# Optimization experiments

Measured on AMD Instinct MI355X. Metric: run time of the kernel, lower is better.

Reference implementation:

```python
import jax, jax.numpy as jnp
import numpy as np

HEADS = 8
DIM_HEAD = 64


def setup_inputs() -> dict:
    key = jax.random.key(0)
    k1, k2, k3 = jax.random.split(key, 3)
    B, C, L = 8, 512, 8192
    hidden = HEADS * DIM_HEAD  # 512
    x = jax.random.normal(k1, (B, C, L), dtype=jnp.float32)
    W_qkv = jax.random.normal(k2, (3 * hidden, C), dtype=jnp.float32) * (1.0 / np.sqrt(C))
    W_out = jax.random.normal(k3, (C, hidden), dtype=jnp.float32) * (1.0 / np.sqrt(hidden))
    b_out = jnp.zeros((C,), dtype=jnp.float32)
    return {"x": x, "W_qkv": W_qkv, "W_out": W_out, "b_out": b_out}


def reference(x, W_qkv, W_out, b_out):
    b, c, l = x.shape
    h, d = HEADS, DIM_HEAD
    # pointwise conv1d == channel matmul: [3*h*d, c] x [b, c, l] -> [b, 3*h*d, l]
    qkv = jnp.einsum('oc,bcl->bol', W_qkv, x)
    q, k, v = jnp.split(qkv, 3, axis=1)
    q = q.reshape(b, h, d, l)
    k = jax.nn.softmax(k.reshape(b, h, d, l), axis=-1)
    v = v.reshape(b, h, d, l)
    # context = k @ v^T : [b,h,d,d]
    context = jnp.einsum('bhdl,bhel->bhde', k, v)
    # out = context^T @ q : [b,h,e,l]
    out = jnp.einsum('bhde,bhdl->bhel', context, q)
    out = out.reshape(b, h * d, l)
    # to_out pointwise conv with bias
    return jnp.einsum('ch,bhl->bcl', W_out, out) + b_out[None, :, None]
```

## Files before the change

### kernel.cpp

```cpp
#include <hip/hip_runtime.h>
#include <hip/hip_bf16.h>

typedef unsigned short u16;
typedef __attribute__((ext_vector_type(8))) short s16x8;
typedef __attribute__((ext_vector_type(4))) float f32x4;

__device__ __forceinline__ u16 f2bf(float f) {
  union { float f; unsigned u; } v; v.f = f;
  unsigned r = (v.u + 0x7fffu + ((v.u >> 16) & 1u)) >> 16;
  return (u16)r;
}
__device__ __forceinline__ float bf2f(u16 u) {
  union { unsigned u; float f; } v; v.u = ((unsigned)u) << 16;
  return v.f;
}
__device__ __forceinline__ void gld_lds16(const void* g, void* l) {
  __builtin_amdgcn_global_load_lds(
      (const __attribute__((address_space(1))) void*)g,
      (__attribute__((address_space(3))) void*)l, 16, 0, 0);
}
__device__ __forceinline__ s16x8 dsr128(const u16* p) {
  s16x8 r;
  asm volatile("ds_read_b128 %0, %1"
               : "=v"(r)
               : "v"((const __attribute__((address_space(3))) u16*)p));
  return r;
}

__global__ void prep_w(const float* __restrict__ Wqkv, const float* __restrict__ Woutf,
                       u16* __restrict__ Wkv, u16* __restrict__ WqT, u16* __restrict__ Wout) {
  int i = blockIdx.x * 256 + threadIdx.x;
  Wkv[i] = f2bf(Wqkv[262144 + i]);
  if (i < 262144) {
    int c = i >> 9, o = i & 511;
    WqT[i]  = f2bf(Wqkv[o * 512 + c]);
    Wout[i] = f2bf(Woutf[i]);
  }
}

__global__ __launch_bounds__(256) void prep_x(const float* __restrict__ x, u16* __restrict__ xt) {
  __shared__ float t[32][33];
  int l0 = blockIdx.x * 32, c0 = blockIdx.y * 32;
  size_t b = blockIdx.z;
  int tid = threadIdx.x;
  int r = tid >> 3, q = tid & 7;
  const float4 v = *(const float4*)(x + (b * 512 + c0 + r) * 8192 + l0 + q * 4);
  t[r][q * 4 + 0] = v.x; t[r][q * 4 + 1] = v.y;
  t[r][q * 4 + 2] = v.z; t[r][q * 4 + 3] = v.w;
  __syncthreads();
  ushort4 o;
  o.x = f2bf(t[q * 4 + 0][r]); o.y = f2bf(t[q * 4 + 1][r]);
  o.z = f2bf(t[q * 4 + 2][r]); o.w = f2bf(t[q * 4 + 3][r]);
  *(ushort4*)(xt + (b * 8192 + l0 + r) * 512 + c0 + q * 4) = o;
}

__global__ __launch_bounds__(256) void gemm_bt(
    const u16* __restrict__ A, size_t sA,
    const u16* __restrict__ BT, size_t sB,
    u16* __restrict__ Cv, size_t sC,
    int N, int K)
{
  __shared__ u16 lsa[128 * 32];
  __shared__ u16 lsb[128 * 32];
  int tid = threadIdx.x, wid = tid >> 6, lane = tid & 63;
  int m0 = blockIdx.y << 7, n0 = blockIdx.x << 7;
  const u16* Ab = A + (size_t)blockIdx.z * sA;
  const u16* Bb = BT + (size_t)blockIdx.z * sB;
  int fr = lane & 15, kg = lane >> 4;
  int wr = wid >> 1, wc = wid & 1;
  int f0 = tid, f1 = tid + 256;
  const u16* pA0 = Ab + (size_t)(m0 + (f0 >> 2)) * K + (f0 & 3) * 8;
  const u16* pA1 = Ab + (size_t)(m0 + (f1 >> 2)) * K + (f1 & 3) * 8;
  const u16* pB0 = Bb + (size_t)(n0 + (f0 >> 2)) * K + (f0 & 3) * 8;
  const u16* pB1 = Bb + (size_t)(n0 + (f1 >> 2)) * K + (f1 & 3) * 8;
  u16* dA0 = &lsa[wid * 512];
  u16* dA1 = &lsa[(wid + 4) * 512];
  u16* dB0 = &lsb[wid * 512];
  u16* dB1 = &lsb[(wid + 4) * 512];
  f32x4 acc[4][4] = {};
  for (int kt = 0; kt < K; kt += 32) {
    gld_lds16(pA0, dA0); gld_lds16(pA1, dA1);
    gld_lds16(pB0, dB0); gld_lds16(pB1, dB1);
    pA0 += 32; pA1 += 32; pB0 += 32; pB1 += 32;
    __syncthreads();
    s16x8 af[4], bf_[4];
#pragma unroll
    for (int mi = 0; mi < 4; ++mi)
      af[mi] = *(const s16x8*)&lsa[(wr * 64 + mi * 16 + fr) * 32 + kg * 8];
#pragma unroll
    for (int ni = 0; ni < 4; ++ni)
      bf_[ni] = *(const s16x8*)&lsb[(wc * 64 + ni * 16 + fr) * 32 + kg * 8];
#pragma unroll
    for (int mi = 0; mi < 4; ++mi)
#pragma unroll
      for (int ni = 0; ni < 4; ++ni)
        acc[mi][ni] = __builtin_amdgcn_mfma_f32_16x16x32_bf16(af[mi], bf_[ni], acc[mi][ni], 0, 0, 0);
    __syncthreads();
  }
  int r0 = m0 + wr * 64 + kg * 4;
  int c0 = n0 + wc * 64 + fr;
  u16* C = Cv + (size_t)blockIdx.z * sC;
#pragma unroll
  for (int mi = 0; mi < 4; ++mi)
#pragma unroll
    for (int ni = 0; ni < 4; ++ni)
#pragma unroll
      for (int j = 0; j < 4; ++j)
        C[(size_t)(r0 + mi * 16 + j) * N + (c0 + ni * 16)] = f2bf(acc[mi][ni][j]);
}

template <int OUTF>
__global__ __launch_bounds__(256, 3) void gemm128(
    const u16* __restrict__ A, size_t sA,
    const u16* __restrict__ BT, size_t sB,
    void* __restrict__ Cv, size_t sC,
    const float* __restrict__ bias,
    int Mt, int Nt)
{
  __shared__ u16 lsa[3][4096];
  __shared__ u16 lsb[3][4096];
  const int tid = threadIdx.x, wid = tid >> 6, lane = tid & 63;
  const int fr = lane & 15, kg = lane >> 4;
  const int wr = wid >> 1, wc = wid & 1;

  const int nwg = (int)gridDim.x;
  const int bx = (int)blockIdx.x;
  const int id = (bx & 7) * (nwg >> 3) + (bx >> 3);
  const int my = id % Mt;
  const int t2 = id / Mt;
  const int nx = t2 % Nt;
  const int z  = t2 / Nt;
  const int m0 = my << 7, n0 = nx << 7;
  const u16* Ab = A + (size_t)z * sA;
  const u16* Bb = BT + (size_t)z * sB;

  const int P0 = tid, P1 = tid + 256;
  int b2_, s_, t_;
  b2_ = P0 >> 3; s_ = P0 & 7; t_ = (s_ - b2_) & 7;
  const size_t g0 = (size_t)((b2_ << 1) + (t_ >> 2)) * 512 + (t_ & 3) * 8;
  b2_ = P1 >> 3; s_ = P1 & 7; t_ = (s_ - b2_) & 7;
  const size_t g1 = (size_t)((b2_ << 1) + (t_ >> 2)) * 512 + (t_ & 3) * 8;
  const u16* paG0 = Ab + (size_t)m0 * 512 + g0;
  const u16* paG1 = Ab + (size_t)m0 * 512 + g1;
  const u16* pbG0 = Bb + (size_t)n0 * 512 + g0;
  const u16* pbG1 = Bb + (size_t)n0 * 512 + g1;

  int aoff[4], boff[4];
#pragma unroll
  for (int i = 0; i < 4; ++i) {
    int ra = wr * 64 + i * 16 + fr;
    aoff[i] = (ra >> 1) * 64 + ((((ra & 1) << 2) + kg + (ra >> 1)) & 7) * 8;
    int rb = wc * 64 + i * 16 + fr;
    boff[i] = (rb >> 1) * 64 + ((((rb & 1) << 2) + kg + (rb >> 1)) & 7) * 8;
  }

  auto stage = [&](int sl, int kt) {
    gld_lds16(paG0 + kt, &lsa[sl][P0 * 8]);
    gld_lds16(paG1 + kt, &lsa[sl][P1 * 8]);
    gld_lds16(pbG0 + kt, &lsb[sl][P0 * 8]);
    gld_lds16(pbG1 + kt, &lsb[sl][P1 * 8]);
  };

  f32x4 acc[4][4] = {};
  stage(0, 0);
  stage(1, 32);
#pragma unroll
  for (int k = 0; k < 16; ++k) {
    if (k < 14) stage((k + 2) % 3, (k + 2) * 32);
    if (k < 14)      { asm volatile("s_waitcnt vmcnt(8)" ::: "memory"); }
    else if (k == 14){ asm volatile("s_waitcnt vmcnt(4)" ::: "memory"); }
    else             { asm volatile("s_waitcnt vmcnt(0)" ::: "memory"); }
    __builtin_amdgcn_s_barrier();
    s16x8 af[4], bf_[4];
    const u16* la = lsa[k % 3];
    const u16* lb = lsb[k % 3];
#pragma unroll
    for (int mi = 0; mi < 4; ++mi) af[mi] = dsr128(la + aoff[mi]);
#pragma unroll
    for (int ni = 0; ni < 4; ++ni) bf_[ni] = dsr128(lb + boff[ni]);
    asm volatile("s_waitcnt lgkmcnt(0)" ::: "memory");
    __builtin_amdgcn_sched_barrier(0);
    __builtin_amdgcn_s_setprio(1);
#pragma unroll
    for (int mi = 0; mi < 4; ++mi)
#pragma unroll
      for (int ni = 0; ni < 4; ++ni)
        acc[mi][ni] = __builtin_amdgcn_mfma_f32_16x16x32_bf16(af[mi], bf_[ni], acc[mi][ni], 0, 0, 0);
    __builtin_amdgcn_s_setprio(0);
    __builtin_amdgcn_s_barrier();
  }

  const int r0 = m0 + wr * 64 + kg * 4;
  const int c0 = n0 + wc * 64 + fr;
  if (OUTF == 0) {
    u16* C = (u16*)Cv + (size_t)z * sC;
#pragma unroll
    for (int mi = 0; mi < 4; ++mi)
#pragma unroll
      for (int ni = 0; ni < 4; ++ni)
#pragma unroll
        for (int j = 0; j < 4; ++j)
          C[(size_t)(r0 + mi * 16 + j) * 8192 + (c0 + ni * 16)] = f2bf(acc[mi][ni][j]);
  } else {
    float* C = (float*)Cv + (size_t)z * sC;
#pragma unroll
    for (int mi = 0; mi < 4; ++mi)
#pragma unroll
      for (int j = 0; j < 4; ++j) {
        float bv = bias[r0 + mi * 16 + j];
#pragma unroll
        for (int ni = 0; ni < 4; ++ni)
          C[(size_t)(r0 + mi * 16 + j) * 8192 + (c0 + ni * 16)] = acc[mi][ni][j] + bv;
      }
  }
}

#define NSPLIT 16
#define SLICE  512
__global__ __launch_bounds__(256) void ctx_partial(const u16* __restrict__ kv,
                                                   float* __restrict__ E, float* __restrict__ Z) {
  int s = blockIdx.x, h = blockIdx.y, b = blockIdx.z;
  int tid = threadIdx.x, wid = tid >> 6, lane = tid & 63;
  int fr = lane & 15, kg = lane >> 4;
  const u16* kbase = kv + ((size_t)b * 1024 + h * 64) * 8192;
  const u16* vbase = kbase + (size_t)512 * 8192;
  int d = wid * 16 + fr;
  const u16* krow = kbase + (size_t)d * 8192 + s * SLICE + kg * 8;
  f32x4 acc[4] = {};
  float z = 0.f;
  for (int l = 0; l < SLICE; l += 32) {
    s16x8 kf = *(const s16x8*)(krow + l);
    s16x8 pf;
#pragma unroll
    for (int j = 0; j < 8; ++j) {
      float p = __expf(bf2f((u16)kf[j]));
      z += p;
      pf[j] = (short)f2bf(p);
    }
#pragma unroll
    for (int ni = 0; ni < 4; ++ni) {
      int e = ni * 16 + fr;
      const s16x8 vf = *(const s16x8*)(vbase + (size_t)e * 8192 + s * SLICE + kg * 8 + l);
      acc[ni] = __builtin_amdgcn_mfma_f32_16x16x32_bf16(pf, vf, acc[ni], 0, 0, 0);
    }
  }
  z += __shfl_xor(z, 16);
  z += __shfl_xor(z, 32);
  size_t bh = (size_t)(b * 8 + h);
  if (kg == 0) atomicAdd(&Z[bh * 64 + d], z);
  float* Eb = E + bh * 4096;
#pragma unroll
  for (int ni = 0; ni < 4; ++ni)
#pragma unroll
    for (int j = 0; j < 4; ++j)
      atomicAdd(&Eb[(wid * 16 + kg * 4 + j) * 64 + ni * 16 + fr], acc[ni][j]);
}

__global__ __launch_bounds__(256) void m1_fused(const float* __restrict__ E, const float* __restrict__ Z,
                                                const u16* __restrict__ Wout, u16* __restrict__ M1) {
  int cb = blockIdx.x, h = blockIdx.y, b = blockIdx.z;
  __shared__ float ctx[64][65];
  __shared__ float zs[64];
  int tid = threadIdx.x;
  size_t bh = (size_t)(b * 8 + h);
  const float* Eb = E + bh * 4096;
  if (tid < 64) zs[tid] = Z[bh * 64 + tid];
  __syncthreads();
  for (int i = tid; i < 4096; i += 256)
    ctx[i >> 6][i & 63] = Eb[i] / zs[i >> 6];
  __syncthreads();
  int d = tid & 63;
  int hbase = h * 64;
  for (int ci = 0; ci < 16; ++ci) {
    int c = __builtin_amdgcn_readfirstlane(cb * 64 + (tid >> 6) + ci * 4);
    const u16* wrow = Wout + c * 512 + hbase;
    float a0 = 0.f, a1 = 0.f, a2 = 0.f, a3 = 0.f;
#pragma unroll
    for (int e = 0; e < 64; e += 4) {
      a0 += bf2f(wrow[e + 0]) * ctx[d][e + 0];
      a1 += bf2f(wrow[e + 1]) * ctx[d][e + 1];
      a2 += bf2f(wrow[e + 2]) * ctx[d][e + 2];
      a3 += bf2f(wrow[e + 3]) * ctx[d][e + 3];
    }
    M1[((size_t)b * 512 + c) * 512 + hbase + d] = f2bf((a0 + a1) + (a2 + a3));
  }
}

extern "C" void kernel_launch(void* const* d_in, const int* in_sizes, int n_in,
                              void* d_out, int out_size, void* d_ws, size_t ws_size,
                              hipStream_t stream) {
  const float* x     = (const float*)d_in[0];
  const float* Wqkv  = (const float*)d_in[1];
  const float* Woutf = (const float*)d_in[2];
  const float* bout  = (const float*)d_in[3];
  char* ws = (char*)d_ws;
  u16*  xt  = (u16*)ws;
  u16*  kv  = (u16*)(ws + 67108864);
  u16*  Wkv = (u16*)(ws + 201326592);
  u16*  WqT = (u16*)(ws + 202375168);
  u16*  Wo  = (u16*)(ws + 202899456);
  u16*  M1  = (u16*)(ws + 203423744);
  u16*  G   = (u16*)(ws + 207618048);
  float* E  = (float*)(ws + 211812352);
  float* Z  = (float*)(ws + 212860928);

  hipMemsetAsync(ws + 211812352, 0, 1048576 + 16384, stream);
  prep_w<<<2048, 256, 0, stream>>>(Wqkv, Woutf, Wkv, WqT, Wo);
  prep_x<<<dim3(256, 16, 8), 256, 0, stream>>>(x, xt);
  gemm128<0><<<4096, 256, 0, stream>>>(Wkv, 0, xt, (size_t)8192 * 512,
                                       kv, (size_t)1024 * 8192, nullptr, 8, 64);
  ctx_partial<<<dim3(NSPLIT, 8, 8), 256, 0, stream>>>(kv, E, Z);
  m1_fused<<<dim3(8, 8, 8), 256, 0, stream>>>(E, Z, Wo, M1);
  gemm_bt<<<dim3(4, 4, 8), 256, 0, stream>>>(M1, (size_t)512 * 512, WqT, 0,
                                             G, (size_t)512 * 512, 512, 512);
  gemm128<1><<<2048, 256, 0, stream>>>(G, (size_t)512 * 512, xt, (size_t)8192 * 512,
                                       d_out, (size_t)512 * 8192, bout, 4, 64);
}
```

Measured before the change: 271.9 us.

## Fuse KV projection GEMM with softmax-exp and context accumulation

Reorders the K/V weight rows so each 128-row tile holds one head's 64 K rows and 64 V rows. The new gemm_ctx kernel computes that tile, applies exp to K, and reduces the row sums and the K·V^T partial context in LDS before adding them atomically into E and Z. This removes the 128 MB bf16 kv intermediate write and its re-read by the separate ctx_partial kernel. The cost is many more atomic adds, one set per 128-column tile instead of per 512-column slice, plus an extra LDS epilogue in the GEMM. exp is applied without subtracting a max, as before.

```diff
diff --git a/kernel.cpp b/kernel.cpp
--- a/kernel.cpp
+++ b/kernel.cpp
@@ -28,9 +28,14 @@
 }
 
 __global__ void prep_w(const float* __restrict__ Wqkv, const float* __restrict__ Woutf,
-                       u16* __restrict__ Wkv, u16* __restrict__ WqT, u16* __restrict__ Wout) {
+                       u16* __restrict__ Wkv2, u16* __restrict__ WqT, u16* __restrict__ Wout) {
   int i = blockIdx.x * 256 + threadIdx.x;
-  Wkv[i] = f2bf(Wqkv[262144 + i]);
+  {
+    int o = i >> 9, c = i & 511;
+    int h = o >> 7, r = o & 127;
+    int src = (r < 64) ? (512 + h * 64 + r) : (1024 + h * 64 + (r - 64));
+    Wkv2[i] = f2bf(Wqkv[src * 512 + c]);
+  }
   if (i < 262144) {
     int c = i >> 9, o = i & 511;
     WqT[i]  = f2bf(Wqkv[o * 512 + c]);
@@ -109,11 +114,130 @@
         C[(size_t)(r0 + mi * 16 + j) * N + (c0 + ni * 16)] = f2bf(acc[mi][ni][j]);
 }
 
-template <int OUTF>
-__global__ __launch_bounds__(256, 3) void gemm128(
+__global__ __launch_bounds__(256, 3) void gemm_ctx(
+    const u16* __restrict__ A,
+    const u16* __restrict__ BT, size_t sB,
+    float* __restrict__ E, float* __restrict__ Z)
+{
+  __shared__ u16 pool[24576];
+  const int tid = threadIdx.x, wid = tid >> 6, lane = tid & 63;
+  const int fr = lane & 15, kg = lane >> 4;
+  const int wr = wid >> 1, wc = wid & 1;
+
+  const int nwg = (int)gridDim.x;
+  const int bx = (int)blockIdx.x;
+  const int id = (bx & 7) * (nwg >> 3) + (bx >> 3);
+  const int my = id % 8;
+  const int t2 = id / 8;
+  const int nx = t2 % 64;
+  const int z  = t2 / 64;
+  const int m0 = my << 7, n0 = nx << 7;
+  const u16* Ab = A + (size_t)m0 * 512;
+  const u16* Bb = BT + (size_t)z * sB + (size_t)n0 * 512;
+
+  const int P0 = tid, P1 = tid + 256;
+  int b2_, s_, t_;
+  b2_ = P0 >> 3; s_ = P0 & 7; t_ = (s_ - b2_) & 7;
+  const size_t g0 = (size_t)((b2_ << 1) + (t_ >> 2)) * 512 + (t_ & 3) * 8;
+  b2_ = P1 >> 3; s_ = P1 & 7; t_ = (s_ - b2_) & 7;
+  const size_t g1 = (size_t)((b2_ << 1) + (t_ >> 2)) * 512 + (t_ & 3) * 8;
+
+  int aoff[4], boff[4];
+#pragma unroll
+  for (int i = 0; i < 4; ++i) {
+    int ra = wr * 64 + i * 16 + fr;
+    aoff[i] = (ra >> 1) * 64 + ((((ra & 1) << 2) + kg + (ra >> 1)) & 7) * 8;
+    int rb = wc * 64 + i * 16 + fr;
+    boff[i] = (rb >> 1) * 64 + ((((rb & 1) << 2) + kg + (rb >> 1)) & 7) * 8;
+  }
+
+  auto stage = [&](int sl, int kt) {
+    gld_lds16(Ab + g0 + kt, &pool[sl * 4096 + P0 * 8]);
+    gld_lds16(Ab + g1 + kt, &pool[sl * 4096 + P1 * 8]);
+    gld_lds16(Bb + g0 + kt, &pool[12288 + sl * 4096 + P0 * 8]);
+    gld_lds16(Bb + g1 + kt, &pool[12288 + sl * 4096 + P1 * 8]);
+  };
+
+  f32x4 acc[4][4] = {};
+  stage(0, 0);
+  stage(1, 32);
+#pragma unroll
+  for (int k = 0; k < 16; ++k) {
+    if (k < 14) stage((k + 2) % 3, (k + 2) * 32);
+    if (k < 14)      { asm volatile("s_waitcnt vmcnt(8)" ::: "memory"); }
+    else if (k == 14){ asm volatile("s_waitcnt vmcnt(4)" ::: "memory"); }
+    else             { asm volatile("s_waitcnt vmcnt(0)" ::: "memory"); }
+    __builtin_amdgcn_s_barrier();
+    s16x8 af[4], bf_[4];
+    const u16* la = &pool[(k % 3) * 4096];
+    const u16* lb = &pool[12288 + (k % 3) * 4096];
+#pragma unroll
+    for (int mi = 0; mi < 4; ++mi) af[mi] = dsr128(la + aoff[mi]);
+#pragma unroll
+    for (int ni = 0; ni < 4; ++ni) bf_[ni] = dsr128(lb + boff[ni]);
+    asm volatile("s_waitcnt lgkmcnt(0)" ::: "memory");
+    __builtin_amdgcn_sched_barrier(0);
+    __builtin_amdgcn_s_setprio(1);
+#pragma unroll
+    for (int mi = 0; mi < 4; ++mi)
+#pragma unroll
+      for (int ni = 0; ni < 4; ++ni)
+        acc[mi][ni] = __builtin_amdgcn_mfma_f32_16x16x32_bf16(af[mi], bf_[ni], acc[mi][ni], 0, 0, 0);
+    __builtin_amdgcn_s_setprio(0);
+    __builtin_amdgcn_s_barrier();
+  }
+
+  const size_t bh = (size_t)z * 8 + my;
+  u16* kbuf = pool;
+  u16* vbuf = pool + 64 * 136;
+#pragma unroll
+  for (int mi = 0; mi < 4; ++mi)
+#pragma unroll
+    for (int ni = 0; ni < 4; ++ni)
+#pragma unroll
+      for (int j = 0; j < 4; ++j) {
+        int r = mi * 16 + kg * 4 + j;
+        int l = wc * 64 + ni * 16 + fr;
+        float vv = acc[mi][ni][j];
+        if (wr == 0) kbuf[r * 136 + l] = f2bf(__expf(vv));
+        else         vbuf[r * 136 + l] = f2bf(vv);
+      }
+  __syncthreads();
+  {
+    int d = tid >> 2, q = tid & 3;
+    float s = 0.f;
+#pragma unroll
+    for (int i = 0; i < 4; ++i) {
+      s16x8 k8 = *(const s16x8*)&kbuf[d * 136 + q * 32 + i * 8];
+#pragma unroll
+      for (int j = 0; j < 8; ++j) s += bf2f((u16)k8[j]);
+    }
+    s += __shfl_xor(s, 1);
+    s += __shfl_xor(s, 2);
+    if (q == 0) atomicAdd(&Z[bh * 64 + d], s);
+  }
+  f32x4 eacc[4] = {};
+#pragma unroll
+  for (int ks = 0; ks < 4; ++ks) {
+    s16x8 ka = *(const s16x8*)&kbuf[(wid * 16 + fr) * 136 + ks * 32 + kg * 8];
+#pragma unroll
+    for (int n2 = 0; n2 < 4; ++n2) {
+      s16x8 vb = *(const s16x8*)&vbuf[(n2 * 16 + fr) * 136 + ks * 32 + kg * 8];
+      eacc[n2] = __builtin_amdgcn_mfma_f32_16x16x32_bf16(ka, vb, eacc[n2], 0, 0, 0);
+    }
+  }
+  float* Eb = E + bh * 4096;
+#pragma unroll
+  for (int n2 = 0; n2 < 4; ++n2)
+#pragma unroll
+    for (int j = 0; j < 4; ++j)
+      atomicAdd(&Eb[(wid * 16 + kg * 4 + j) * 64 + n2 * 16 + fr], eacc[n2][j]);
+}
+
+__global__ __launch_bounds__(256, 3) void gemm128f(
     const u16* __restrict__ A, size_t sA,
     const u16* __restrict__ BT, size_t sB,
-    void* __restrict__ Cv, size_t sC,
+    float* __restrict__ Cv, size_t sC,
     const float* __restrict__ bias,
     int Mt, int Nt)
 {
@@ -192,68 +316,16 @@
 
   const int r0 = m0 + wr * 64 + kg * 4;
   const int c0 = n0 + wc * 64 + fr;
-  if (OUTF == 0) {
-    u16* C = (u16*)Cv + (size_t)z * sC;
-#pragma unroll
-    for (int mi = 0; mi < 4; ++mi)
+  float* C = Cv + (size_t)z * sC;
+#pragma unroll
+  for (int mi = 0; mi < 4; ++mi)
+#pragma unroll
+    for (int j = 0; j < 4; ++j) {
+      float bv = bias[r0 + mi * 16 + j];
 #pragma unroll
       for (int ni = 0; ni < 4; ++ni)
-#pragma unroll
-        for (int j = 0; j < 4; ++j)
-          C[(size_t)(r0 + mi * 16 + j) * 8192 + (c0 + ni * 16)] = f2bf(acc[mi][ni][j]);
-  } else {
-    float* C = (float*)Cv + (size_t)z * sC;
-#pragma unroll
-    for (int mi = 0; mi < 4; ++mi)
-#pragma unroll
-      for (int j = 0; j < 4; ++j) {
-        float bv = bias[r0 + mi * 16 + j];
-#pragma unroll
-        for (int ni = 0; ni < 4; ++ni)
-          C[(size_t)(r0 + mi * 16 + j) * 8192 + (c0 + ni * 16)] = acc[mi][ni][j] + bv;
-      }
-  }
-}
-
-#define NSPLIT 16
-#define SLICE  512
-__global__ __launch_bounds__(256) void ctx_partial(const u16* __restrict__ kv,
-                                                   float* __restrict__ E, float* __restrict__ Z) {
-  int s = blockIdx.x, h = blockIdx.y, b = blockIdx.z;
-  int tid = threadIdx.x, wid = tid >> 6, lane = tid & 63;
-  int fr = lane & 15, kg = lane >> 4;
-  const u16* kbase = kv + ((size_t)b * 1024 + h * 64) * 8192;
-  const u16* vbase = kbase + (size_t)512 * 8192;
-  int d = wid * 16 + fr;
-  const u16* krow = kbase + (size_t)d * 8192 + s * SLICE + kg * 8;
-  f32x4 acc[4] = {};
-  float z = 0.f;
-  for (int l = 0; l < SLICE; l += 32) {
-    s16x8 kf = *(const s16x8*)(krow + l);
-    s16x8 pf;
-#pragma unroll
-    for (int j = 0; j < 8; ++j) {
-      float p = __expf(bf2f((u16)kf[j]));
-      z += p;
-      pf[j] = (short)f2bf(p);
+        C[(size_t)(r0 + mi * 16 + j) * 8192 + (c0 + ni * 16)] = acc[mi][ni][j] + bv;
     }
-#pragma unroll
-    for (int ni = 0; ni < 4; ++ni) {
-      int e = ni * 16 + fr;
-      const s16x8 vf = *(const s16x8*)(vbase + (size_t)e * 8192 + s * SLICE + kg * 8 + l);
-      acc[ni] = __builtin_amdgcn_mfma_f32_16x16x32_bf16(pf, vf, acc[ni], 0, 0, 0);
-    }
-  }
-  z += __shfl_xor(z, 16);
-  z += __shfl_xor(z, 32);
-  size_t bh = (size_t)(b * 8 + h);
-  if (kg == 0) atomicAdd(&Z[bh * 64 + d], z);
-  float* Eb = E + bh * 4096;
-#pragma unroll
-  for (int ni = 0; ni < 4; ++ni)
-#pragma unroll
-    for (int j = 0; j < 4; ++j)
-      atomicAdd(&Eb[(wid * 16 + kg * 4 + j) * 64 + ni * 16 + fr], acc[ni][j]);
 }
 
 __global__ __launch_bounds__(256) void m1_fused(const float* __restrict__ E, const float* __restrict__ Z,
@@ -295,8 +367,7 @@
   const float* bout  = (const float*)d_in[3];
   char* ws = (char*)d_ws;
   u16*  xt  = (u16*)ws;
-  u16*  kv  = (u16*)(ws + 67108864);
-  u16*  Wkv = (u16*)(ws + 201326592);
+  u16*  Wkv2= (u16*)(ws + 201326592);
   u16*  WqT = (u16*)(ws + 202375168);
   u16*  Wo  = (u16*)(ws + 202899456);
   u16*  M1  = (u16*)(ws + 203423744);
@@ -305,14 +376,12 @@
   float* Z  = (float*)(ws + 212860928);
 
   hipMemsetAsync(ws + 211812352, 0, 1048576 + 16384, stream);
-  prep_w<<<2048, 256, 0, stream>>>(Wqkv, Woutf, Wkv, WqT, Wo);
+  prep_w<<<2048, 256, 0, stream>>>(Wqkv, Woutf, Wkv2, WqT, Wo);
   prep_x<<<dim3(256, 16, 8), 256, 0, stream>>>(x, xt);
-  gemm128<0><<<4096, 256, 0, stream>>>(Wkv, 0, xt, (size_t)8192 * 512,
-                                       kv, (size_t)1024 * 8192, nullptr, 8, 64);
-  ctx_partial<<<dim3(NSPLIT, 8, 8), 256, 0, stream>>>(kv, E, Z);
+  gemm_ctx<<<4096, 256, 0, stream>>>(Wkv2, xt, (size_t)8192 * 512, E, Z);
   m1_fused<<<dim3(8, 8, 8), 256, 0, stream>>>(E, Z, Wo, M1);
   gemm_bt<<<dim3(4, 4, 8), 256, 0, stream>>>(M1, (size_t)512 * 512, WqT, 0,
                                              G, (size_t)512 * 512, 512, 512);
-  gemm128<1><<<2048, 256, 0, stream>>>(G, (size_t)512 * 512, xt, (size_t)8192 * 512,
-                                       d_out, (size_t)512 * 8192, bout, 4, 64);
-}
+  gemm128f<<<2048, 256, 0, stream>>>(G, (size_t)512 * 512, xt, (size_t)8192 * 512,
+                                     (float*)d_out, (size_t)512 * 8192, bout, 4, 64);
+}
```

Measured after the change: 228.0 us. -16.1%, faster.
